# Kernel optimization log

Hardware: AMD Instinct MI355X
Metric: run time of the kernel (lower is better)

The kernel has to match this reference:

```python
import jax, jax.numpy as jnp
import numpy as np

N = 8192       # nodes
E = 131072     # edges
R = 4          # relations
IN_EMBD = 64   # per-feature embedding dim -> node feat = 6*64 = 384
H1 = 256       # layer_embd
D = 128        # out_embd; layer2 outputs 2*D
VOCABS = [35, 10, 5, 7, 5, 5]


def setup_inputs() -> dict:
    key = jax.random.key(0)
    ks = jax.random.split(key, 20)
    inp = {}
    inp['x'] = jax.random.randint(ks[0], (N, 6), 0, 5)
    inp['edge_index'] = jax.random.randint(ks[1], (2, E), 0, N)
    inp['edge_type'] = jax.random.randint(ks[2], (E,), 0, R)
    for i, v in enumerate(VOCABS):
        inp[f'emb{i}'] = jax.random.normal(ks[3 + i], (v, IN_EMBD), jnp.float32) * 0.1
    inp['W1'] = jax.random.normal(ks[10], (R, 6 * IN_EMBD, H1), jnp.float32) * 0.05
    inp['root1'] = jax.random.normal(ks[11], (6 * IN_EMBD, H1), jnp.float32) * 0.05
    inp['b1'] = jnp.zeros((H1,), jnp.float32)
    inp['W2'] = jax.random.normal(ks[12], (R, H1, 2 * D), jnp.float32) * 0.05
    inp['root2'] = jax.random.normal(ks[13], (H1, 2 * D), jnp.float32) * 0.05
    inp['b2'] = jnp.zeros((2 * D,), jnp.float32)
    return inp


def _rgcn(h, W, root, b, src, dst, edge_type):
    # RGCNConv (PyG semantics): out_i = root h_i + b + sum_r mean_{j in N_r(i)} W_r h_j
    out = h @ root + b
    for r in range(R):
        hr = h @ W[r]                                   # [N, out]
        m = (edge_type == r).astype(h.dtype)            # [E]
        s = jax.ops.segment_sum(hr[src] * m[:, None], dst, num_segments=N)
        c = jax.ops.segment_sum(m, dst, num_segments=N)
        out = out + s / jnp.clip(c, 1.0)[:, None]
    return out


def reference(x, edge_index, edge_type, emb0, emb1, emb2, emb3, emb4, emb5,
              W1, root1, b1, W2, root2, b2):
    embs = [emb0, emb1, emb2, emb3, emb4, emb5]
    x_ = jnp.concatenate([embs[i][x[:, i]] for i in range(6)], axis=1)  # [N, 384]
    src, dst = edge_index[0], edge_index[1]
    h1 = jax.nn.sigmoid(_rgcn(x_, W1, root1, b1, src, dst, edge_type))
    h2 = jax.nn.sigmoid(_rgcn(h1, W2, root2, b2, src, dst, edge_type))
    mu, logvar = h2[:, :D], h2[:, D:]
    std = jnp.exp(0.5 * logvar)
    eps = jax.random.normal(jax.random.key(42), std.shape, std.dtype)
    Z = eps * std + mu                                   # reparametrize
    A_hat = jax.nn.sigmoid(Z @ Z.T)                      # [N, N]
    A = jnp.zeros((N, N), jnp.float32).at[src, dst].set(1.0)
    return A, A_hat, mu, logvar
```

## Files before the change

kernel.cpp:

```cpp
#include <hip/hip_runtime.h>
#include <hip/hip_bf16.h>
#include <cstdint>
#include <cstddef>

#define N_NODES 8192
#define NE      131072
#define NR      4
#define NC      1280

typedef __attribute__((ext_vector_type(8))) short bf16x8;
typedef __attribute__((ext_vector_type(4))) float f32x4;

__device__ __forceinline__ float sigmoidf_(float x) {
  return 1.0f / (1.0f + __expf(-x));
}

__device__ __forceinline__ void split_bf16(float v, __hip_bfloat16& hi, __hip_bfloat16& lo) {
  hi = __float2bfloat16(v);
  lo = __float2bfloat16(v - __bfloat162float(hi));
}

__global__ void k_embed(const int* __restrict__ xi,
                        const float* __restrict__ e0, const float* __restrict__ e1,
                        const float* __restrict__ e2, const float* __restrict__ e3,
                        const float* __restrict__ e4, const float* __restrict__ e5,
                        __hip_bfloat16* __restrict__ xhi) {
  int n = blockIdx.x;
  int c = threadIdx.x;
  int i = c >> 6, d = c & 63;
  const float* t;
  switch (i) {
    case 0: t = e0; break; case 1: t = e1; break; case 2: t = e2; break;
    case 3: t = e3; break; case 4: t = e4; break; default: t = e5; break;
  }
  float v = t[(size_t)xi[n * 6 + i] * 64 + d];
  xhi[(size_t)n * 384 + c] = __float2bfloat16(v);
}

template<int LO>
__global__ void k_pack_t(const float* __restrict__ root, const float* __restrict__ W,
                         __hip_bfloat16* __restrict__ bhi, __hip_bfloat16* __restrict__ blo,
                         int K) {
  int k = blockIdx.x, seg = blockIdx.y, c = threadIdx.x;
  float v = (seg == 0) ? root[(size_t)k * 256 + c]
                       : W[((size_t)(seg - 1) * K + k) * 256 + c];
  int n = seg * 256 + c;
  if (LO) {
    __hip_bfloat16 h, l; split_bf16(v, h, l);
    bhi[(size_t)n * K + k] = h;
    blo[(size_t)n * K + k] = l;
  } else {
    bhi[(size_t)n * K + k] = __float2bfloat16(v);
  }
}

template<int SPLIT3, int ACT, int SYM>
__global__ __launch_bounds__(256) void k_gemm2(
    const ushort* __restrict__ Ahi, const ushort* __restrict__ Alo,
    const ushort* __restrict__ Bhi, const ushort* __restrict__ Blo,
    float* __restrict__ C, int Nc, int K) {
  __shared__ ushort Bs[(SPLIT3 ? 2 : 1) * 128 * 128];
  ushort* BsH = Bs;
  ushort* BsL = Bs + 128 * 128;

  const int tid = threadIdx.x;
  const int w = tid >> 6, l = tid & 63;
  const int lrow = l & 15, lk8 = (l >> 4) * 8;

  int brow, bcol, p = 0, q = 0;
  if (SYM) {
    int b = blockIdx.x;
    q = (int)((sqrtf(8.f * (float)b + 1.f) - 1.f) * 0.5f);
    while ((q + 1) * (q + 2) / 2 <= b) ++q;
    while (q * (q + 1) / 2 > b) --q;
    p = b - q * (q + 1) / 2;
    brow = p * 128; bcol = q * 128;
  } else {
    brow = blockIdx.y * 128; bcol = blockIdx.x * 128;
  }

  f32x4 acc[2][8] = {};
  const size_t arow0 = (size_t)(brow + w * 32 + lrow) * K + lk8;
  const size_t arow1 = arow0 + (size_t)16 * K;

  for (int kc = 0; kc < K; kc += 128) {
    bf16x8 aH[4][2], aL[4][2];
#pragma unroll
    for (int kk = 0; kk < 4; ++kk) {
      aH[kk][0] = *(const bf16x8*)(Ahi + arow0 + kc + kk * 32);
      aH[kk][1] = *(const bf16x8*)(Ahi + arow1 + kc + kk * 32);
      if (SPLIT3) {
        aL[kk][0] = *(const bf16x8*)(Alo + arow0 + kc + kk * 32);
        aL[kk][1] = *(const bf16x8*)(Alo + arow1 + kc + kk * 32);
      }
    }
    if (kc) __syncthreads();
#pragma unroll
    for (int it = 0; it < 8; ++it) {
      int o = (it * 256 + tid) * 16;
      int row = o >> 8, sb = o & 255;
      int se = (sb ^ ((row & 7) << 4)) >> 1;
      size_t g = (size_t)(bcol + row) * K + kc + se;
      *(uint4*)((char*)BsH + o) = *(const uint4*)(Bhi + g);
      if (SPLIT3) *(uint4*)((char*)BsL + o) = *(const uint4*)(Blo + g);
    }
    __syncthreads();
#pragma unroll
    for (int kk = 0; kk < 4; ++kk) {
#pragma unroll
      for (int n = 0; n < 8; ++n) {
        int row_t = n * 16 + lrow;
        int addr = row_t * 256 + ((kk * 64 + (l >> 4) * 16) ^ ((row_t & 7) << 4));
        bf16x8 b_h = *(const bf16x8*)((const char*)BsH + addr);
        acc[0][n] = __builtin_amdgcn_mfma_f32_16x16x32_bf16(aH[kk][0], b_h, acc[0][n], 0, 0, 0);
        acc[1][n] = __builtin_amdgcn_mfma_f32_16x16x32_bf16(aH[kk][1], b_h, acc[1][n], 0, 0, 0);
        if (SPLIT3) {
          bf16x8 b_l = *(const bf16x8*)((const char*)BsL + addr);
          acc[0][n] = __builtin_amdgcn_mfma_f32_16x16x32_bf16(aL[kk][0], b_h, acc[0][n], 0, 0, 0);
          acc[1][n] = __builtin_amdgcn_mfma_f32_16x16x32_bf16(aL[kk][1], b_h, acc[1][n], 0, 0, 0);
          acc[0][n] = __builtin_amdgcn_mfma_f32_16x16x32_bf16(aH[kk][0], b_l, acc[0][n], 0, 0, 0);
          acc[1][n] = __builtin_amdgcn_mfma_f32_16x16x32_bf16(aH[kk][1], b_l, acc[1][n], 0, 0, 0);
        }
      }
    }
  }

  const int crow = (l >> 4) * 4, ccol = l & 15;
#pragma unroll
  for (int m = 0; m < 2; ++m)
#pragma unroll
    for (int n = 0; n < 8; ++n) {
      float v[4];
#pragma unroll
      for (int r = 0; r < 4; ++r) {
        float t = acc[m][n][r];
        v[r] = ACT ? sigmoidf_(t) : t;
      }
      int rloc = w * 32 + m * 16 + crow;
      int cloc = n * 16 + ccol;
      float* cp = C + (size_t)(brow + rloc) * Nc + bcol + cloc;
#pragma unroll
      for (int r = 0; r < 4; ++r) cp[(size_t)r * Nc] = v[r];
      if (SYM && p != q) {
        float* mp = C + (size_t)(bcol + cloc) * Nc + brow + rloc;
        *(float4*)mp = make_float4(v[0], v[1], v[2], v[3]);
      }
    }
}

__global__ void k_zerof4(float4* __restrict__ p, size_t n4) {
  size_t i = (size_t)blockIdx.x * blockDim.x + threadIdx.x;
  size_t stride = (size_t)gridDim.x * blockDim.x;
  float4 z = make_float4(0.f, 0.f, 0.f, 0.f);
  for (; i < n4; i += stride) p[i] = z;
}
__global__ void k_zero_i(int* __restrict__ p, int n) {
  int i = blockIdx.x * 256 + threadIdx.x;
  if (i < n) p[i] = 0;
}

__global__ void k_count(const int* __restrict__ dst, int* __restrict__ deg) {
  int e = blockIdx.x * 256 + threadIdx.x;
  if (e < NE) atomicAdd(&deg[dst[e]], 1);
}

__global__ __launch_bounds__(1024) void k_scan(const int* __restrict__ deg,
                                               int* __restrict__ off) {
  __shared__ int s[1024];
  int t = threadIdx.x;
  int v[8];
  int run = 0;
#pragma unroll
  for (int i = 0; i < 8; ++i) {
    int tmp = deg[t * 8 + i];
    v[i] = run; run += tmp;
  }
  s[t] = run;
  __syncthreads();
  for (int ofs = 1; ofs < 1024; ofs <<= 1) {
    int x = (t >= ofs) ? s[t - ofs] : 0;
    __syncthreads();
    s[t] += x;
    __syncthreads();
  }
  int base = (t > 0) ? s[t - 1] : 0;
#pragma unroll
  for (int i = 0; i < 8; ++i) off[t * 8 + i] = base + v[i];
  if (t == 1023) off[8192] = base + run;
}

__global__ void k_fill(const int* __restrict__ src, const int* __restrict__ dst,
                       const int* __restrict__ et, const int* __restrict__ off,
                       int* __restrict__ cursor, int* __restrict__ csr) {
  int e = blockIdx.x * 256 + threadIdx.x;
  if (e < NE) {
    int d = dst[e];
    int pos = atomicAdd(&cursor[d], 1);
    csr[off[d] + pos] = (src[e] << 2) | et[e];
  }
}

template<int LAYER>
__global__ __launch_bounds__(256) void k_combine(
    const float* __restrict__ hall, const float* __restrict__ bias,
    const int* __restrict__ off, const int* __restrict__ csr,
    __hip_bfloat16* __restrict__ h_hi, __hip_bfloat16* __restrict__ h_lo,
    float* __restrict__ muo, float* __restrict__ lvo) {
  __shared__ int sc[64];
  int n = blockIdx.x, c = threadIdx.x;
  int beg = off[n], end = off[n + 1];
  float a0 = 0.f, a1 = 0.f, a2 = 0.f, a3 = 0.f;
  int c0 = 0, c1 = 0, c2 = 0, c3 = 0;
  for (int base = beg; base < end; base += 64) {
    int mcnt = min(64, end - base);
    if (c < 64 && base + c < end) sc[c] = csr[base + c];
    __syncthreads();
    int i = 0;
    for (; i + 4 <= mcnt; i += 4) {
      int p0 = sc[i], p1 = sc[i + 1], p2 = sc[i + 2], p3 = sc[i + 3];
      float v0 = hall[(size_t)(p0 >> 2) * NC + 256 + (size_t)(p0 & 3) * 256 + c];
      float v1 = hall[(size_t)(p1 >> 2) * NC + 256 + (size_t)(p1 & 3) * 256 + c];
      float v2 = hall[(size_t)(p2 >> 2) * NC + 256 + (size_t)(p2 & 3) * 256 + c];
      float v3 = hall[(size_t)(p3 >> 2) * NC + 256 + (size_t)(p3 & 3) * 256 + c];
      int r;
      r = p0 & 3; if (r == 0) { a0 += v0; ++c0; } else if (r == 1) { a1 += v0; ++c1; }
                  else if (r == 2) { a2 += v0; ++c2; } else { a3 += v0; ++c3; }
      r = p1 & 3; if (r == 0) { a0 += v1; ++c0; } else if (r == 1) { a1 += v1; ++c1; }
                  else if (r == 2) { a2 += v1; ++c2; } else { a3 += v1; ++c3; }
      r = p2 & 3; if (r == 0) { a0 += v2; ++c0; } else if (r == 1) { a1 += v2; ++c1; }
                  else if (r == 2) { a2 += v2; ++c2; } else { a3 += v2; ++c3; }
      r = p3 & 3; if (r == 0) { a0 += v3; ++c0; } else if (r == 1) { a1 += v3; ++c1; }
                  else if (r == 2) { a2 += v3; ++c2; } else { a3 += v3; ++c3; }
    }
    for (; i < mcnt; ++i) {
      int pp = sc[i];
      int r = pp & 3;
      float v = hall[(size_t)(pp >> 2) * NC + 256 + (size_t)r * 256 + c];
      if (r == 0) { a0 += v; ++c0; } else if (r == 1) { a1 += v; ++c1; }
      else if (r == 2) { a2 += v; ++c2; } else { a3 += v; ++c3; }
    }
    __syncthreads();
  }
  float v = hall[(size_t)n * NC + c] + bias[c]
          + a0 / (float)max(c0, 1) + a1 / (float)max(c1, 1)
          + a2 / (float)max(c2, 1) + a3 / (float)max(c3, 1);
  float sg = sigmoidf_(v);
  if (LAYER == 1) {
    __hip_bfloat16 h, l; split_bf16(sg, h, l);
    h_hi[(size_t)n * 256 + c] = h;
    h_lo[(size_t)n * 256 + c] = l;
  } else {
    if (c < 128) muo[(size_t)n * 128 + c] = sg;
    else         lvo[(size_t)n * 128 + (c - 128)] = sg;
  }
}

__device__ __forceinline__ float bits_to_normal(unsigned bits) {
  float f = __uint_as_float((bits >> 9) | 0x3f800000u) - 1.0f;
  const float lo = -0.99999994f;
  float u = __fadd_rn(__fmul_rn(f, 2.0f), lo);
  u = fmaxf(lo, u);
  float w = -log1pf(-u * u);
  float p;
  if (w < 5.0f) {
    w = w - 2.5f;
    p = 2.81022636e-08f;
    p = fmaf(p, w, 3.43273939e-07f);
    p = fmaf(p, w, -3.5233877e-06f);
    p = fmaf(p, w, -4.39150654e-06f);
    p = fmaf(p, w, 0.00021858087f);
    p = fmaf(p, w, -0.00125372503f);
    p = fmaf(p, w, -0.00417768164f);
    p = fmaf(p, w, 0.246640727f);
    p = fmaf(p, w, 1.50140941f);
  } else {
    w = sqrtf(w) - 3.0f;
    p = -0.000200214257f;
    p = fmaf(p, w, 0.000100950558f);
    p = fmaf(p, w, 0.00134934322f);
    p = fmaf(p, w, -0.00367342844f);
    p = fmaf(p, w, 0.00573950773f);
    p = fmaf(p, w, -0.0076224613f);
    p = fmaf(p, w, 0.00943887047f);
    p = fmaf(p, w, 1.00167406f);
    p = fmaf(p, w, 2.83297682f);
  }
  return 1.41421356f * (p * u);
}

__global__ void k_z(const float* __restrict__ mu, const float* __restrict__ lv,
                    __hip_bfloat16* __restrict__ zhi, __hip_bfloat16* __restrict__ zlo) {
  unsigned j = blockIdx.x * 256 + threadIdx.x;
  const unsigned ks0 = 0u, ks1 = 42u, ks2 = 0x1BD11BDAu ^ 0u ^ 42u;
  unsigned x0 = 0u + ks0;
  unsigned x1 = j + ks1;
#define RND(r) { x0 += x1; x1 = (x1 << r) | (x1 >> (32 - r)); x1 ^= x0; }
  RND(13) RND(15) RND(26) RND(6)  x0 += ks1; x1 += ks2 + 1u;
  RND(17) RND(29) RND(16) RND(24) x0 += ks2; x1 += ks0 + 2u;
  RND(13) RND(15) RND(26) RND(6)  x0 += ks0; x1 += ks1 + 3u;
  RND(17) RND(29) RND(16) RND(24) x0 += ks1; x1 += ks2 + 4u;
  RND(13) RND(15) RND(26) RND(6)  x0 += ks2; x1 += ks0 + 5u;
#undef RND
  unsigned bits = x0 ^ x1;
  float e = bits_to_normal(bits);
  float z = fmaf(e, __expf(0.5f * lv[j]), mu[j]);
  __hip_bfloat16 h, l; split_bf16(z, h, l);
  zhi[j] = h; zlo[j] = l;
}

__global__ void k_scatterA(const int* __restrict__ src, const int* __restrict__ dst,
                           float* __restrict__ A) {
  int e = blockIdx.x * 256 + threadIdx.x;
  if (e < NE) A[(size_t)src[e] * N_NODES + dst[e]] = 1.0f;
}

extern "C" void kernel_launch(void* const* d_in, const int* in_sizes, int n_in,
                              void* d_out, int out_size, void* d_ws, size_t ws_size,
                              hipStream_t stream) {
  const int* x    = (const int*)d_in[0];
  const int* ei   = (const int*)d_in[1];
  const int* src  = ei;
  const int* dst  = ei + NE;
  const int* et   = (const int*)d_in[2];
  const float* e0 = (const float*)d_in[3];
  const float* e1 = (const float*)d_in[4];
  const float* e2 = (const float*)d_in[5];
  const float* e3 = (const float*)d_in[6];
  const float* e4 = (const float*)d_in[7];
  const float* e5 = (const float*)d_in[8];
  const float* W1 = (const float*)d_in[9];
  const float* r1 = (const float*)d_in[10];
  const float* b1 = (const float*)d_in[11];
  const float* W2 = (const float*)d_in[12];
  const float* r2 = (const float*)d_in[13];
  const float* b2 = (const float*)d_in[14];

  float* out  = (float*)d_out;
  float* A    = out;
  float* Ahat = out + (size_t)N_NODES * N_NODES;
  float* muo  = Ahat + (size_t)N_NODES * N_NODES;
  float* lvo  = muo + (size_t)N_NODES * 128;

  char* wp = (char*)d_ws;
  auto carve = [&](size_t bytes) { char* r = wp; wp += (bytes + 255) & ~(size_t)255; return r; };
  __hip_bfloat16* xhi  = (__hip_bfloat16*)carve((size_t)8192 * 384 * 2);
  __hip_bfloat16* bthi = (__hip_bfloat16*)carve((size_t)NC * 384 * 2);
  __hip_bfloat16* btlo = (__hip_bfloat16*)carve((size_t)NC * 384 * 2);
  float*          hall = (float*)carve((size_t)8192 * NC * 4);
  __hip_bfloat16* h1hi = (__hip_bfloat16*)carve((size_t)8192 * 256 * 2);
  __hip_bfloat16* h1lo = (__hip_bfloat16*)carve((size_t)8192 * 256 * 2);
  __hip_bfloat16* zhi  = (__hip_bfloat16*)carve((size_t)8192 * 128 * 2);
  __hip_bfloat16* zlo  = (__hip_bfloat16*)carve((size_t)8192 * 128 * 2);
  int*            deg  = (int*)carve((size_t)8192 * 4);
  int*            cur  = (int*)carve((size_t)8192 * 4);
  int*            off  = (int*)carve((size_t)8193 * 4);
  int*            csr  = (int*)carve((size_t)NE * 4);

  k_zero_i<<<64, 256, 0, stream>>>(deg, 16384);
  k_count<<<NE / 256, 256, 0, stream>>>(dst, deg);
  k_scan<<<1, 1024, 0, stream>>>(deg, off);
  k_fill<<<NE / 256, 256, 0, stream>>>(src, dst, et, off, cur, csr);

  k_embed<<<8192, 384, 0, stream>>>(x, e0, e1, e2, e3, e4, e5, xhi);
  k_pack_t<0><<<dim3(384, 5), 256, 0, stream>>>(r1, W1, bthi, nullptr, 384);
  k_gemm2<0, 0, 0><<<dim3(NC / 128, 64), 256, 0, stream>>>(
      (const ushort*)xhi, nullptr, (const ushort*)bthi, nullptr, hall, NC, 384);
  k_combine<1><<<8192, 256, 0, stream>>>(hall, b1, off, csr, h1hi, h1lo, nullptr, nullptr);

  k_pack_t<1><<<dim3(256, 5), 256, 0, stream>>>(r2, W2, bthi, btlo, 256);
  k_gemm2<1, 0, 0><<<dim3(NC / 128, 64), 256, 0, stream>>>(
      (const ushort*)h1hi, (const ushort*)h1lo, (const ushort*)bthi, (const ushort*)btlo,
      hall, NC, 256);
  k_combine<2><<<8192, 256, 0, stream>>>(hall, b2, off, csr, nullptr, nullptr, muo, lvo);

  k_z<<<4096, 256, 0, stream>>>(muo, lvo, zhi, zlo);

  k_zerof4<<<8192, 256, 0, stream>>>((float4*)A, (size_t)N_NODES * N_NODES / 4);
  k_scatterA<<<NE / 256, 256, 0, stream>>>(src, dst, A);

  k_gemm2<1, 1, 1><<<dim3(64 * 65 / 2), 256, 0, stream>>>(
      (const ushort*)zhi, (const ushort*)zlo, (const ushort*)zhi, (const ushort*)zlo,
      Ahat, N_NODES, 128);
}
```

Measured before the change: 356.7 us.

## Aggregate neighbor features before the transform and fuse bias/sigmoid into the GEMM

Reorders each RGCN layer to take per-relation neighbor means of the input features first. Each layer then runs as a single GEMM with the concatenated [self | mean_r] operand and the stacked root/W weights, instead of a GEMM to a wide 1280-column intermediate followed by a gather-combine pass. Bias and sigmoid move into the GEMM epilogue, so the large fp32 hall buffer and its gathers go away. The cost is a larger K dimension (1920 and 1280) with narrower output tiles (64 columns, 4x64 grid). Layer 2 keeps its bf16 hi/lo split for both the aggregated operand and the weights, and the gather in layer 1 now reads 384-wide bf16 rows.

New measurement: 419.2 us. 17.5% more time.

```diff
diff --git a/kernel.cpp b/kernel.cpp
--- a/kernel.cpp
+++ b/kernel.cpp
@@ -6,7 +6,6 @@
 #define N_NODES 8192
 #define NE      131072
 #define NR      4
-#define NC      1280
 
 typedef __attribute__((ext_vector_type(8))) short bf16x8;
 typedef __attribute__((ext_vector_type(4))) float f32x4;
@@ -15,16 +14,24 @@
   return 1.0f / (1.0f + __expf(-x));
 }
 
-__device__ __forceinline__ void split_bf16(float v, __hip_bfloat16& hi, __hip_bfloat16& lo) {
-  hi = __float2bfloat16(v);
-  lo = __float2bfloat16(v - __bfloat162float(hi));
+__device__ __forceinline__ ushort f2b(float v) {
+  __hip_bfloat16 h = __float2bfloat16(v);
+  return *(ushort*)&h;
+}
+__device__ __forceinline__ float b2f(ushort u) {
+  __hip_bfloat16 h = *(__hip_bfloat16*)&u;
+  return __bfloat162float(h);
+}
+__device__ __forceinline__ void split2(float v, ushort& hi, ushort& lo) {
+  hi = f2b(v);
+  lo = f2b(v - b2f(hi));
 }
 
 __global__ void k_embed(const int* __restrict__ xi,
                         const float* __restrict__ e0, const float* __restrict__ e1,
                         const float* __restrict__ e2, const float* __restrict__ e3,
                         const float* __restrict__ e4, const float* __restrict__ e5,
-                        __hip_bfloat16* __restrict__ xhi) {
+                        ushort* __restrict__ A1) {
   int n = blockIdx.x;
   int c = threadIdx.x;
   int i = c >> 6, d = c & 63;
@@ -34,24 +41,228 @@
     case 3: t = e3; break; case 4: t = e4; break; default: t = e5; break;
   }
   float v = t[(size_t)xi[n * 6 + i] * 64 + d];
-  xhi[(size_t)n * 384 + c] = __float2bfloat16(v);
+  A1[(size_t)n * 1920 + c] = f2b(v);
 }
 
 template<int LO>
 __global__ void k_pack_t(const float* __restrict__ root, const float* __restrict__ W,
-                         __hip_bfloat16* __restrict__ bhi, __hip_bfloat16* __restrict__ blo,
-                         int K) {
+                         ushort* __restrict__ bhi, ushort* __restrict__ blo, int K) {
   int k = blockIdx.x, seg = blockIdx.y, c = threadIdx.x;
   float v = (seg == 0) ? root[(size_t)k * 256 + c]
                        : W[((size_t)(seg - 1) * K + k) * 256 + c];
-  int n = seg * 256 + c;
+  size_t idx = (size_t)c * (5 * K) + seg * K + k;
   if (LO) {
-    __hip_bfloat16 h, l; split_bf16(v, h, l);
-    bhi[(size_t)n * K + k] = h;
-    blo[(size_t)n * K + k] = l;
+    ushort h, l; split2(v, h, l);
+    bhi[idx] = h; blo[idx] = l;
   } else {
-    bhi[(size_t)n * K + k] = __float2bfloat16(v);
-  }
+    bhi[idx] = f2b(v);
+  }
+}
+
+__global__ void k_zero_i(int* __restrict__ p, int n) {
+  int i = blockIdx.x * 256 + threadIdx.x;
+  if (i < n) p[i] = 0;
+}
+__global__ void k_count(const int* __restrict__ dst, int* __restrict__ deg) {
+  int e = blockIdx.x * 256 + threadIdx.x;
+  if (e < NE) atomicAdd(&deg[dst[e]], 1);
+}
+__global__ __launch_bounds__(1024) void k_scan(const int* __restrict__ deg,
+                                               int* __restrict__ off) {
+  __shared__ int s[1024];
+  int t = threadIdx.x;
+  int v[8];
+  int run = 0;
+#pragma unroll
+  for (int i = 0; i < 8; ++i) {
+    int tmp = deg[t * 8 + i];
+    v[i] = run; run += tmp;
+  }
+  s[t] = run;
+  __syncthreads();
+  for (int ofs = 1; ofs < 1024; ofs <<= 1) {
+    int x = (t >= ofs) ? s[t - ofs] : 0;
+    __syncthreads();
+    s[t] += x;
+    __syncthreads();
+  }
+  int base = (t > 0) ? s[t - 1] : 0;
+#pragma unroll
+  for (int i = 0; i < 8; ++i) off[t * 8 + i] = base + v[i];
+  if (t == 1023) off[8192] = base + run;
+}
+__global__ void k_fill(const int* __restrict__ src, const int* __restrict__ dst,
+                       const int* __restrict__ et, const int* __restrict__ off,
+                       int* __restrict__ cursor, int* __restrict__ csr) {
+  int e = blockIdx.x * 256 + threadIdx.x;
+  if (e < NE) {
+    int d = dst[e];
+    int pos = atomicAdd(&cursor[d], 1);
+    csr[off[d] + pos] = (src[e] << 2) | et[e];
+  }
+}
+
+__global__ __launch_bounds__(384) void k_agg1(const ushort* __restrict__ A1r,
+                                              const int* __restrict__ off,
+                                              const int* __restrict__ csr,
+                                              ushort* __restrict__ A1w) {
+  __shared__ int sc[64];
+  int n = blockIdx.x, c = threadIdx.x;
+  int beg = off[n], end = off[n + 1];
+  float a0 = 0.f, a1 = 0.f, a2 = 0.f, a3 = 0.f;
+  int c0 = 0, c1 = 0, c2 = 0, c3 = 0;
+  for (int base = beg; base < end; base += 64) {
+    int m = min(64, end - base);
+    __syncthreads();
+    if (c < 64 && base + c < end) sc[c] = csr[base + c];
+    __syncthreads();
+    for (int i = 0; i < m; ++i) {
+      int p = sc[i];
+      int r = p & 3;
+      float v = b2f(A1r[(size_t)(p >> 2) * 1920 + c]);
+      if (r == 0) { a0 += v; ++c0; } else if (r == 1) { a1 += v; ++c1; }
+      else if (r == 2) { a2 += v; ++c2; } else { a3 += v; ++c3; }
+    }
+  }
+  size_t b = (size_t)n * 1920 + 384;
+  A1w[b + 0 * 384 + c] = f2b(a0 / (float)max(c0, 1));
+  A1w[b + 1 * 384 + c] = f2b(a1 / (float)max(c1, 1));
+  A1w[b + 2 * 384 + c] = f2b(a2 / (float)max(c2, 1));
+  A1w[b + 3 * 384 + c] = f2b(a3 / (float)max(c3, 1));
+}
+
+__global__ __launch_bounds__(256) void k_agg2(const float* __restrict__ h1,
+                                              const int* __restrict__ off,
+                                              const int* __restrict__ csr,
+                                              ushort* __restrict__ agghi,
+                                              ushort* __restrict__ agglo) {
+  __shared__ int sc[64];
+  int n = blockIdx.x, c = threadIdx.x;
+  int beg = off[n], end = off[n + 1];
+  float a0 = 0.f, a1 = 0.f, a2 = 0.f, a3 = 0.f;
+  int c0 = 0, c1 = 0, c2 = 0, c3 = 0;
+  for (int base = beg; base < end; base += 64) {
+    int m = min(64, end - base);
+    __syncthreads();
+    if (c < 64 && base + c < end) sc[c] = csr[base + c];
+    __syncthreads();
+    for (int i = 0; i < m; ++i) {
+      int p = sc[i];
+      int r = p & 3;
+      float v = h1[(size_t)(p >> 2) * 256 + c];
+      if (r == 0) { a0 += v; ++c0; } else if (r == 1) { a1 += v; ++c1; }
+      else if (r == 2) { a2 += v; ++c2; } else { a3 += v; ++c3; }
+    }
+  }
+  float m0 = a0 / (float)max(c0, 1), m1 = a1 / (float)max(c1, 1);
+  float m2 = a2 / (float)max(c2, 1), m3 = a3 / (float)max(c3, 1);
+  size_t b = (size_t)n * 1024;
+  ushort h, l;
+  split2(m0, h, l); agghi[b + 0 * 256 + c] = h; agglo[b + 0 * 256 + c] = l;
+  split2(m1, h, l); agghi[b + 1 * 256 + c] = h; agglo[b + 1 * 256 + c] = l;
+  split2(m2, h, l); agghi[b + 2 * 256 + c] = h; agglo[b + 2 * 256 + c] = l;
+  split2(m3, h, l); agghi[b + 3 * 256 + c] = h; agglo[b + 3 * 256 + c] = l;
+}
+
+template<int LAYER>
+__global__ __launch_bounds__(256) void k_gemm_l(
+    const ushort* __restrict__ A1,
+    const ushort* __restrict__ h1hi, const ushort* __restrict__ h1lo,
+    const ushort* __restrict__ agghi, const ushort* __restrict__ agglo,
+    const ushort* __restrict__ Bhi, const ushort* __restrict__ Blo,
+    const float* __restrict__ bias,
+    float* __restrict__ oh1f, ushort* __restrict__ oh1hi, ushort* __restrict__ oh1lo,
+    float* __restrict__ muo, float* __restrict__ lvo) {
+  constexpr int K = (LAYER == 1) ? 1920 : 1280;
+  constexpr int SPLIT3 = (LAYER == 2) ? 1 : 0;
+  __shared__ ushort Bs[(SPLIT3 ? 2 : 1) * 64 * 128];
+  ushort* BsH = Bs;
+  ushort* BsL = Bs + 64 * 128;
+
+  const int tid = threadIdx.x;
+  const int w = tid >> 6, l = tid & 63;
+  const int lrow = l & 15, lk8 = (l >> 4) * 8;
+  const int brow = blockIdx.y * 128, bcol = blockIdx.x * 64;
+
+  f32x4 acc[2][4] = {};
+  const int r0 = brow + w * 32 + lrow;
+
+  for (int kc = 0; kc < K; kc += 128) {
+    bf16x8 aH[4][2], aL[4][2];
+#pragma unroll
+    for (int kk = 0; kk < 4; ++kk) {
+      int kg = kc + kk * 32 + lk8;
+      if (LAYER == 1) {
+        aH[kk][0] = *(const bf16x8*)(A1 + (size_t)r0 * 1920 + kg);
+        aH[kk][1] = *(const bf16x8*)(A1 + (size_t)(r0 + 16) * 1920 + kg);
+      } else {
+        if (kc < 256) {
+          aH[kk][0] = *(const bf16x8*)(h1hi + (size_t)r0 * 256 + kg);
+          aH[kk][1] = *(const bf16x8*)(h1hi + (size_t)(r0 + 16) * 256 + kg);
+          aL[kk][0] = *(const bf16x8*)(h1lo + (size_t)r0 * 256 + kg);
+          aL[kk][1] = *(const bf16x8*)(h1lo + (size_t)(r0 + 16) * 256 + kg);
+        } else {
+          int ka = kg - 256;
+          aH[kk][0] = *(const bf16x8*)(agghi + (size_t)r0 * 1024 + ka);
+          aH[kk][1] = *(const bf16x8*)(agghi + (size_t)(r0 + 16) * 1024 + ka);
+          aL[kk][0] = *(const bf16x8*)(agglo + (size_t)r0 * 1024 + ka);
+          aL[kk][1] = *(const bf16x8*)(agglo + (size_t)(r0 + 16) * 1024 + ka);
+        }
+      }
+    }
+    if (kc) __syncthreads();
+#pragma unroll
+    for (int it = 0; it < 4; ++it) {
+      int o = (it * 256 + tid) * 16;
+      int row = o >> 8, sb = o & 255;
+      int se = (sb ^ ((row & 7) << 4)) >> 1;
+      size_t g = (size_t)(bcol + row) * K + kc + se;
+      *(uint4*)((char*)BsH + o) = *(const uint4*)(Bhi + g);
+      if (SPLIT3) *(uint4*)((char*)BsL + o) = *(const uint4*)(Blo + g);
+    }
+    __syncthreads();
+#pragma unroll
+    for (int kk = 0; kk < 4; ++kk) {
+#pragma unroll
+      for (int n = 0; n < 4; ++n) {
+        int row_t = n * 16 + lrow;
+        int addr = row_t * 256 + ((kk * 64 + (l >> 4) * 16) ^ ((row_t & 7) << 4));
+        bf16x8 b_h = *(const bf16x8*)((const char*)BsH + addr);
+        acc[0][n] = __builtin_amdgcn_mfma_f32_16x16x32_bf16(aH[kk][0], b_h, acc[0][n], 0, 0, 0);
+        acc[1][n] = __builtin_amdgcn_mfma_f32_16x16x32_bf16(aH[kk][1], b_h, acc[1][n], 0, 0, 0);
+        if (SPLIT3) {
+          bf16x8 b_l = *(const bf16x8*)((const char*)BsL + addr);
+          acc[0][n] = __builtin_amdgcn_mfma_f32_16x16x32_bf16(aL[kk][0], b_h, acc[0][n], 0, 0, 0);
+          acc[1][n] = __builtin_amdgcn_mfma_f32_16x16x32_bf16(aL[kk][1], b_h, acc[1][n], 0, 0, 0);
+          acc[0][n] = __builtin_amdgcn_mfma_f32_16x16x32_bf16(aH[kk][0], b_l, acc[0][n], 0, 0, 0);
+          acc[1][n] = __builtin_amdgcn_mfma_f32_16x16x32_bf16(aH[kk][1], b_l, acc[1][n], 0, 0, 0);
+        }
+      }
+    }
+  }
+
+  const int crow = (l >> 4) * 4, ccol = l & 15;
+#pragma unroll
+  for (int m = 0; m < 2; ++m)
+#pragma unroll
+    for (int n = 0; n < 4; ++n) {
+      int col = bcol + n * 16 + ccol;
+      float bv = bias[col];
+#pragma unroll
+      for (int r = 0; r < 4; ++r) {
+        int row = brow + w * 32 + m * 16 + crow + r;
+        float sg = sigmoidf_(acc[m][n][r] + bv);
+        if (LAYER == 1) {
+          oh1f[(size_t)row * 256 + col] = sg;
+          ushort h, lo2; split2(sg, h, lo2);
+          oh1hi[(size_t)row * 256 + col] = h;
+          oh1lo[(size_t)row * 256 + col] = lo2;
+        } else {
+          if (col < 128) muo[(size_t)row * 128 + col] = sg;
+          else           lvo[(size_t)row * 128 + col - 128] = sg;
+        }
+      }
+    }
 }
 
 template<int SPLIT3, int ACT, int SYM>
@@ -153,106 +364,6 @@
   size_t stride = (size_t)gridDim.x * blockDim.x;
   float4 z = make_float4(0.f, 0.f, 0.f, 0.f);
   for (; i < n4; i += stride) p[i] = z;
-}
-__global__ void k_zero_i(int* __restrict__ p, int n) {
-  int i = blockIdx.x * 256 + threadIdx.x;
-  if (i < n) p[i] = 0;
-}
-
-__global__ void k_count(const int* __restrict__ dst, int* __restrict__ deg) {
-  int e = blockIdx.x * 256 + threadIdx.x;
-  if (e < NE) atomicAdd(&deg[dst[e]], 1);
-}
-
-__global__ __launch_bounds__(1024) void k_scan(const int* __restrict__ deg,
-                                               int* __restrict__ off) {
-  __shared__ int s[1024];
-  int t = threadIdx.x;
-  int v[8];
-  int run = 0;
-#pragma unroll
-  for (int i = 0; i < 8; ++i) {
-    int tmp = deg[t * 8 + i];
-    v[i] = run; run += tmp;
-  }
-  s[t] = run;
-  __syncthreads();
-  for (int ofs = 1; ofs < 1024; ofs <<= 1) {
-    int x = (t >= ofs) ? s[t - ofs] : 0;
-    __syncthreads();
-    s[t] += x;
-    __syncthreads();
-  }
-  int base = (t > 0) ? s[t - 1] : 0;
-#pragma unroll
-  for (int i = 0; i < 8; ++i) off[t * 8 + i] = base + v[i];
-  if (t == 1023) off[8192] = base + run;
-}
-
-__global__ void k_fill(const int* __restrict__ src, const int* __restrict__ dst,
-                       const int* __restrict__ et, const int* __restrict__ off,
-                       int* __restrict__ cursor, int* __restrict__ csr) {
-  int e = blockIdx.x * 256 + threadIdx.x;
-  if (e < NE) {
-    int d = dst[e];
-    int pos = atomicAdd(&cursor[d], 1);
-    csr[off[d] + pos] = (src[e] << 2) | et[e];
-  }
-}
-
-template<int LAYER>
-__global__ __launch_bounds__(256) void k_combine(
-    const float* __restrict__ hall, const float* __restrict__ bias,
-    const int* __restrict__ off, const int* __restrict__ csr,
-    __hip_bfloat16* __restrict__ h_hi, __hip_bfloat16* __restrict__ h_lo,
-    float* __restrict__ muo, float* __restrict__ lvo) {
-  __shared__ int sc[64];
-  int n = blockIdx.x, c = threadIdx.x;
-  int beg = off[n], end = off[n + 1];
-  float a0 = 0.f, a1 = 0.f, a2 = 0.f, a3 = 0.f;
-  int c0 = 0, c1 = 0, c2 = 0, c3 = 0;
-  for (int base = beg; base < end; base += 64) {
-    int mcnt = min(64, end - base);
-    if (c < 64 && base + c < end) sc[c] = csr[base + c];
-    __syncthreads();
-    int i = 0;
-    for (; i + 4 <= mcnt; i += 4) {
-      int p0 = sc[i], p1 = sc[i + 1], p2 = sc[i + 2], p3 = sc[i + 3];
-      float v0 = hall[(size_t)(p0 >> 2) * NC + 256 + (size_t)(p0 & 3) * 256 + c];
-      float v1 = hall[(size_t)(p1 >> 2) * NC + 256 + (size_t)(p1 & 3) * 256 + c];
-      float v2 = hall[(size_t)(p2 >> 2) * NC + 256 + (size_t)(p2 & 3) * 256 + c];
-      float v3 = hall[(size_t)(p3 >> 2) * NC + 256 + (size_t)(p3 & 3) * 256 + c];
-      int r;
-      r = p0 & 3; if (r == 0) { a0 += v0; ++c0; } else if (r == 1) { a1 += v0; ++c1; }
-                  else if (r == 2) { a2 += v0; ++c2; } else { a3 += v0; ++c3; }
-      r = p1 & 3; if (r == 0) { a0 += v1; ++c0; } else if (r == 1) { a1 += v1; ++c1; }
-                  else if (r == 2) { a2 += v1; ++c2; } else { a3 += v1; ++c3; }
-      r = p2 & 3; if (r == 0) { a0 += v2; ++c0; } else if (r == 1) { a1 += v2; ++c1; }
-                  else if (r == 2) { a2 += v2; ++c2; } else { a3 += v2; ++c3; }
-      r = p3 & 3; if (r == 0) { a0 += v3; ++c0; } else if (r == 1) { a1 += v3; ++c1; }
-                  else if (r == 2) { a2 += v3; ++c2; } else { a3 += v3; ++c3; }
-    }
-    for (; i < mcnt; ++i) {
-      int pp = sc[i];
-      int r = pp & 3;
-      float v = hall[(size_t)(pp >> 2) * NC + 256 + (size_t)r * 256 + c];
-      if (r == 0) { a0 += v; ++c0; } else if (r == 1) { a1 += v; ++c1; }
-      else if (r == 2) { a2 += v; ++c2; } else { a3 += v; ++c3; }
-    }
-    __syncthreads();
-  }
-  float v = hall[(size_t)n * NC + c] + bias[c]
-          + a0 / (float)max(c0, 1) + a1 / (float)max(c1, 1)
-          + a2 / (float)max(c2, 1) + a3 / (float)max(c3, 1);
-  float sg = sigmoidf_(v);
-  if (LAYER == 1) {
-    __hip_bfloat16 h, l; split_bf16(sg, h, l);
-    h_hi[(size_t)n * 256 + c] = h;
-    h_lo[(size_t)n * 256 + c] = l;
-  } else {
-    if (c < 128) muo[(size_t)n * 128 + c] = sg;
-    else         lvo[(size_t)n * 128 + (c - 128)] = sg;
-  }
 }
 
 __device__ __forceinline__ float bits_to_normal(unsigned bits) {
@@ -289,7 +400,7 @@
 }
 
 __global__ void k_z(const float* __restrict__ mu, const float* __restrict__ lv,
-                    __hip_bfloat16* __restrict__ zhi, __hip_bfloat16* __restrict__ zlo) {
+                    ushort* __restrict__ zhi, ushort* __restrict__ zlo) {
   unsigned j = blockIdx.x * 256 + threadIdx.x;
   const unsigned ks0 = 0u, ks1 = 42u, ks2 = 0x1BD11BDAu ^ 0u ^ 42u;
   unsigned x0 = 0u + ks0;
@@ -304,7 +415,7 @@
   unsigned bits = x0 ^ x1;
   float e = bits_to_normal(bits);
   float z = fmaf(e, __expf(0.5f * lv[j]), mu[j]);
-  __hip_bfloat16 h, l; split_bf16(z, h, l);
+  ushort h, l; split2(z, h, l);
   zhi[j] = h; zlo[j] = l;
 }
 
@@ -343,35 +454,40 @@
 
   char* wp = (char*)d_ws;
   auto carve = [&](size_t bytes) { char* r = wp; wp += (bytes + 255) & ~(size_t)255; return r; };
-  __hip_bfloat16* xhi  = (__hip_bfloat16*)carve((size_t)8192 * 384 * 2);
-  __hip_bfloat16* bthi = (__hip_bfloat16*)carve((size_t)NC * 384 * 2);
-  __hip_bfloat16* btlo = (__hip_bfloat16*)carve((size_t)NC * 384 * 2);
-  float*          hall = (float*)carve((size_t)8192 * NC * 4);
-  __hip_bfloat16* h1hi = (__hip_bfloat16*)carve((size_t)8192 * 256 * 2);
-  __hip_bfloat16* h1lo = (__hip_bfloat16*)carve((size_t)8192 * 256 * 2);
-  __hip_bfloat16* zhi  = (__hip_bfloat16*)carve((size_t)8192 * 128 * 2);
-  __hip_bfloat16* zlo  = (__hip_bfloat16*)carve((size_t)8192 * 128 * 2);
-  int*            deg  = (int*)carve((size_t)8192 * 4);
-  int*            cur  = (int*)carve((size_t)8192 * 4);
-  int*            off  = (int*)carve((size_t)8193 * 4);
-  int*            csr  = (int*)carve((size_t)NE * 4);
+  char* uni = carve((size_t)2 * 8192 * 1024 * 2);
+  ushort* A1    = (ushort*)uni;
+  ushort* agghi = (ushort*)uni;
+  ushort* agglo = (ushort*)(uni + (size_t)8192 * 1024 * 2);
+  ushort* B1t   = (ushort*)carve((size_t)256 * 1920 * 2);
+  ushort* B2thi = (ushort*)carve((size_t)256 * 1280 * 2);
+  ushort* B2tlo = (ushort*)carve((size_t)256 * 1280 * 2);
+  float*  h1f   = (float*)carve((size_t)8192 * 256 * 4);
+  ushort* h1hi  = (ushort*)carve((size_t)8192 * 256 * 2);
+  ushort* h1lo  = (ushort*)carve((size_t)8192 * 256 * 2);
+  ushort* zhi   = (ushort*)carve((size_t)8192 * 128 * 2);
+  ushort* zlo   = (ushort*)carve((size_t)8192 * 128 * 2);
+  int*    deg   = (int*)carve((size_t)8192 * 4);
+  int*    cur   = (int*)carve((size_t)8192 * 4);
+  int*    off   = (int*)carve((size_t)8193 * 4);
+  int*    csr   = (int*)carve((size_t)NE * 4);
 
   k_zero_i<<<64, 256, 0, stream>>>(deg, 16384);
   k_count<<<NE / 256, 256, 0, stream>>>(dst, deg);
   k_scan<<<1, 1024, 0, stream>>>(deg, off);
   k_fill<<<NE / 256, 256, 0, stream>>>(src, dst, et, off, cur, csr);
 
-  k_embed<<<8192, 384, 0, stream>>>(x, e0, e1, e2, e3, e4, e5, xhi);
-  k_pack_t<0><<<dim3(384, 5), 256, 0, stream>>>(r1, W1, bthi, nullptr, 384);
-  k_gemm2<0, 0, 0><<<dim3(NC / 128, 64), 256, 0, stream>>>(
-      (const ushort*)xhi, nullptr, (const ushort*)bthi, nullptr, hall, NC, 384);
-  k_combine<1><<<8192, 256, 0, stream>>>(hall, b1, off, csr, h1hi, h1lo, nullptr, nullptr);
-
-  k_pack_t<1><<<dim3(256, 5), 256, 0, stream>>>(r2, W2, bthi, btlo, 256);
-  k_gemm2<1, 0, 0><<<dim3(NC / 128, 64), 256, 0, stream>>>(
-      (const ushort*)h1hi, (const ushort*)h1lo, (const ushort*)bthi, (const ushort*)btlo,
-      hall, NC, 256);
-  k_combine<2><<<8192, 256, 0, stream>>>(hall, b2, off, csr, nullptr, nullptr, muo, lvo);
+  k_embed<<<8192, 384, 0, stream>>>(x, e0, e1, e2, e3, e4, e5, A1);
+  k_pack_t<0><<<dim3(384, 5), 256, 0, stream>>>(r1, W1, B1t, nullptr, 384);
+  k_agg1<<<8192, 384, 0, stream>>>(A1, off, csr, A1);
+  k_gemm_l<1><<<dim3(4, 64), 256, 0, stream>>>(
+      A1, nullptr, nullptr, nullptr, nullptr, B1t, nullptr, b1,
+      h1f, h1hi, h1lo, nullptr, nullptr);
+
+  k_pack_t<1><<<dim3(256, 5), 256, 0, stream>>>(r2, W2, B2thi, B2tlo, 256);
+  k_agg2<<<8192, 256, 0, stream>>>(h1f, off, csr, agghi, agglo);
+  k_gemm_l<2><<<dim3(4, 64), 256, 0, stream>>>(
+      nullptr, h1hi, h1lo, agghi, agglo, B2thi, B2tlo, b2,
+      nullptr, nullptr, nullptr, muo, lvo);
 
   k_z<<<4096, 256, 0, stream>>>(muo, lvo, zhi, zlo);
 
@@ -379,6 +495,5 @@
   k_scatterA<<<NE / 256, 256, 0, stream>>>(src, dst, A);
 
   k_gemm2<1, 1, 1><<<dim3(64 * 65 / 2), 256, 0, stream>>>(
-      (const ushort*)zhi, (const ushort*)zlo, (const ushort*)zhi, (const ushort*)zlo,
-      Ahat, N_NODES, 128);
-}
+      zhi, zlo, zhi, zlo, Ahat, N_NODES, 128);
+}
```
